# Kernel tuning notes

Measured on AMD Instinct MI355X. Metric: run time of the kernel, lower is better.

Reference implementation:

```python
import jax, jax.numpy as jnp
import numpy as np

N = 50_000          # nodes
E = 1_600_000       # edges (avg degree 32)
IN = 128            # in_feats
H = 4               # num_heads
F = 32              # out_feats per head
CUTOFF = 4.0        # bessel_cutoff
P = 7               # envelope_exponent + 1
ENV_A = -(P + 1) * (P + 2) / 2.0   # -36
ENV_B = P * (P + 2)                # 63
ENV_C = -P * (P + 1) / 2.0         # -28


def setup_inputs() -> dict:
    key = jax.random.key(0)
    ks = jax.random.split(key, 8)
    x = jax.random.normal(ks[0], (N, IN), dtype=jnp.float32)
    distance = jax.random.uniform(ks[1], (E,), dtype=jnp.float32) * CUTOFF
    W_src = jax.random.normal(ks[2], (H * F, IN), dtype=jnp.float32) * 0.05
    b_src = jnp.zeros((H * F,), dtype=jnp.float32)
    W_dst = jax.random.normal(ks[3], (H * F, IN), dtype=jnp.float32) * 0.05
    b_dst = jnp.zeros((H * F,), dtype=jnp.float32)
    attn = jax.random.normal(ks[4], (1, H, F), dtype=jnp.float32) * 0.1
    prelu_alpha = jnp.full((H,), 0.25, dtype=jnp.float32)
    frequencies = jnp.arange(1.0, H + 1.0, dtype=jnp.float32) * np.pi
    src = jax.random.randint(ks[5], (E,), 0, N, dtype=jnp.int32)
    dst = jax.random.randint(ks[6], (E,), 0, N, dtype=jnp.int32)
    return dict(x=x, distance=distance, W_src=W_src, b_src=b_src,
                W_dst=W_dst, b_dst=b_dst, attn=attn,
                prelu_alpha=prelu_alpha, frequencies=frequencies,
                src=src, dst=dst)


def _bessel_coeff(distance, frequencies):
    # distance: [E] -> d_scaled: [E,1]; frequencies: [H] -> coeff: [E,H]
    d = (distance / CUTOFF)[:, None]
    d_p0 = d ** P
    env = d + ENV_A * d_p0 + ENV_B * (d_p0 * d) + ENV_C * (d_p0 * d * d)
    return env * jnp.sin(frequencies * d)


def reference(x, distance, W_src, b_src, W_dst, b_dst, attn,
              prelu_alpha, frequencies, src, dst):
    n = x.shape[0]
    feat_src = (x @ W_src.T + b_src).reshape(n, H, F)   # [N,H,F]
    feat_dst = (x @ W_dst.T + b_dst).reshape(n, H, F)   # [N,H,F]

    coeff = _bessel_coeff(distance, frequencies)[:, :, None]  # [E,H,1]

    el = feat_src[src]                                  # [E,H,F] gather
    e = (el + feat_dst[dst]) * coeff                    # u_add_v then bessel scale
    e = jnp.where(e >= 0, e, prelu_alpha[None, :, None] * e)  # PReLU per head
    score = jnp.einsum('ehf,hf->eh', e, attn[0])        # [E,H]

    # edge softmax over incoming edges per dst node, per head
    seg_max = jax.ops.segment_max(score, dst, num_segments=n)        # [N,H]
    ex = jnp.exp(score - seg_max[dst])                               # [E,H]
    denom = jax.ops.segment_sum(ex, dst, num_segments=n)             # [N,H]
    a = ex / denom[dst]                                              # [E,H]

    # u_mul_e + scatter-sum aggregation
    msgs = el * a[:, :, None]                                        # [E,H,F]
    rst = jax.ops.segment_sum(msgs, dst, num_segments=n)             # [N,H,F]
    return rst
```

## Files before the change

### kernel.cpp

```cpp
#include <hip/hip_runtime.h>
#include <hip/hip_bf16.h>
#include <math.h>

#define N_NODES 50000
#define E_EDGES 1600000
#define HF 128
#define INV_CUTOFF 0.25f
#define ENV_A -36.0f
#define ENV_B 63.0f
#define ENV_C -28.0f

#define GEMM_BLOCKS ((N_NODES + 63) / 64)
#define REC_CAP 72
#define NBUCK 196
#define BUCK_CAP 8960
#define EPB 6250
#define SPLIT 4
#define LCAP 32

typedef __attribute__((ext_vector_type(8))) short bf16x8;
typedef __attribute__((ext_vector_type(4))) float f32x4;

__device__ __forceinline__ unsigned short f2bf(float f) {
  unsigned u = __float_as_uint(f);
  u += 0x7fffu + ((u >> 16) & 1u);
  return (unsigned short)(u >> 16);
}
__device__ __forceinline__ unsigned pack2(float lo, float hi) {
  return (unsigned)f2bf(lo) | ((unsigned)f2bf(hi) << 16);
}
__device__ __forceinline__ float2 up2(unsigned v) {
  return make_float2(__uint_as_float(v << 16), __uint_as_float(v & 0xffff0000u));
}

__device__ __forceinline__ float2 p2add(float2 a, float2 b) {
  return make_float2(a.x + b.x, a.y + b.y);
}
__device__ __forceinline__ float2 p2fma(float2 a, float2 b, float2 c) {
  return make_float2(fmaf(a.x, b.x, c.x), fmaf(a.y, b.y, c.y));
}
__device__ __forceinline__ float2 p2abs(float2 a) {
  return make_float2(fabsf(a.x), fabsf(a.y));
}
__device__ __forceinline__ float2 p2fmas(float s, float2 b, float2 c) {
  return make_float2(fmaf(s, b.x, c.x), fmaf(s, b.y, c.y));
}

__global__ __launch_bounds__(256) void phase1(
    const float* __restrict__ x, const float* __restrict__ Ws,
    const float* __restrict__ Wd,
    const float* __restrict__ bs, const float* __restrict__ bd,
    unsigned short* __restrict__ fs, float* __restrict__ fd,
    const int* __restrict__ dst, const int* __restrict__ src,
    const float* __restrict__ dist,
    int* __restrict__ bcursor, unsigned* __restrict__ bb_pay,
    unsigned char* __restrict__ bb_loc) {
  __shared__ __align__(16) char smem[65536];

  if (blockIdx.x < GEMM_BLOCKS) {
    unsigned short* wlds = (unsigned short*)smem;

    for (int i = threadIdx.x; i < 4096; i += 256) {
      const int n = i >> 4, c = i & 15;
      const float* Wp = ((n < 128) ? Ws : Wd) + (size_t)(n & 127) * HF + c * 8;
      const float4 v0 = *(const float4*)Wp;
      const float4 v1 = *(const float4*)(Wp + 4);
      uint4 pk;
      pk.x = pack2(v0.x, v0.y); pk.y = pack2(v0.z, v0.w);
      pk.z = pack2(v1.x, v1.y); pk.w = pack2(v1.z, v1.w);
      ((uint4*)wlds)[n * 16 + (c ^ (n & 15))] = pk;
    }

    const int lane = threadIdx.x & 63;
    const int wave = threadIdx.x >> 6;
    const int m = lane & 15;
    const int quad = lane >> 4;
    const int row = blockIdx.x * 64 + wave * 16 + m;
    const int rowc = (row < N_NODES) ? row : (N_NODES - 1);

    union { bf16x8 v; unsigned u[4]; } af[4];
    #pragma unroll
    for (int kt = 0; kt < 4; kt++) {
      const float* xp = x + (size_t)rowc * HF + kt * 32 + quad * 8;
      const float4 u0 = *(const float4*)xp;
      const float4 u1 = *(const float4*)(xp + 4);
      af[kt].u[0] = pack2(u0.x, u0.y); af[kt].u[1] = pack2(u0.z, u0.w);
      af[kt].u[2] = pack2(u1.x, u1.y); af[kt].u[3] = pack2(u1.z, u1.w);
    }

    __syncthreads();

    float accA[16][4];
    #pragma unroll
    for (int nt = 0; nt < 16; nt++) {
      const int nrow = nt * 16 + m;
      f32x4 acc = {0.f, 0.f, 0.f, 0.f};
      #pragma unroll
      for (int kt = 0; kt < 4; kt++) {
        const int pc = (kt * 4 + quad) ^ m;
        const bf16x8 bf = *(const bf16x8*)(wlds + (size_t)nrow * HF + pc * 8);
        acc = __builtin_amdgcn_mfma_f32_16x16x32_bf16(af[kt].v, bf, acc, 0, 0, 0);
      }
      accA[nt][0] = acc[0]; accA[nt][1] = acc[1];
      accA[nt][2] = acc[2]; accA[nt][3] = acc[3];
    }

    __syncthreads();
    unsigned short* fsS = wlds;
    float* fdS = (float*)(wlds + 64 * 136);

    const int rl0 = wave * 16 + quad * 4;
    #pragma unroll
    for (int nt = 0; nt < 16; nt++) {
      const int col = nt * 16 + m;
      if (col < 128) {
        const float bias = bs[col];
        #pragma unroll
        for (int r = 0; r < 4; r++)
          fsS[(rl0 + r) * 136 + col] = f2bf(accA[nt][r] + bias);
      } else {
        const float bias = bd[col - 128];
        #pragma unroll
        for (int r = 0; r < 4; r++)
          fdS[(rl0 + r) * 132 + (col - 128)] = accA[nt][r] + bias;
      }
    }
    __syncthreads();

    for (int c = threadIdx.x; c < 1024; c += 256) {
      const int r = c >> 4, off = (c & 15) * 8;
      const int gr = blockIdx.x * 64 + r;
      if (gr < N_NODES)
        *(uint4*)(fs + (size_t)gr * HF + off) = *(const uint4*)(fsS + r * 136 + off);
    }
    for (int c = threadIdx.x; c < 2048; c += 256) {
      const int r = c >> 5, off = (c & 31) * 4;
      const int gr = blockIdx.x * 64 + r;
      if (gr < N_NODES)
        *(float4*)(fd + (size_t)gr * HF + off) = *(const float4*)(fdS + r * 132 + off);
    }
  } else {
    unsigned* pay_s      = (unsigned*)smem;
    unsigned char* bkt_s = (unsigned char*)(smem + 25000);
    unsigned char* loc_s = (unsigned char*)(smem + 31250);
    int* hist = (int*)(smem + 37504);
    int* loff = hist + NBUCK;
    int* base = loff + NBUCK;
    int* cur  = base + NBUCK;

    const int bb = blockIdx.x - GEMM_BLOCKS;
    for (int t = threadIdx.x; t < NBUCK; t += 256) { hist[t] = 0; cur[t] = 0; }
    __syncthreads();
    const int lo = bb * EPB;
    for (int k = threadIdx.x; k < EPB; k += 256)
      atomicAdd(&hist[dst[lo + k] >> 8], 1);
    __syncthreads();
    if (threadIdx.x == 0) {
      int run = 0;
      for (int j = 0; j < NBUCK; j++) { loff[j] = run; run += hist[j]; }
    }
    __syncthreads();
    for (int t = threadIdx.x; t < NBUCK; t += 256)
      base[t] = atomicAdd(&bcursor[t], hist[t]);
    __syncthreads();
    for (int k = threadIdx.x; k < EPB; k += 256) {
      const int d = dst[lo + k];
      const int b = d >> 8;
      float ds = dist[lo + k] * (INV_CUTOFF * 65536.f);
      unsigned dq = (unsigned)(ds + 0.5f);
      if (dq > 65535u) dq = 65535u;
      const int s = loff[b] + atomicAdd(&cur[b], 1);
      pay_s[s] = (unsigned)src[lo + k] | (dq << 16);
      bkt_s[s] = (unsigned char)b;
      loc_s[s] = (unsigned char)(d & 255);
    }
    __syncthreads();
    for (int s = threadIdx.x; s < EPB; s += 256) {
      const int b = bkt_s[s];
      const int dest = base[b] + (s - loff[b]);
      if (dest < BUCK_CAP) {
        bb_pay[(size_t)b * BUCK_CAP + dest] = pay_s[s];
        bb_loc[(size_t)b * BUCK_CAP + dest] = loc_s[s];
      }
    }
  }
}

__global__ __launch_bounds__(256) void bucket_scatter(
    const int* __restrict__ bcursor, const unsigned* __restrict__ bb_pay,
    const unsigned char* __restrict__ bb_loc,
    int* __restrict__ counts, unsigned* __restrict__ rec) {
  __shared__ int cnt[256];
  __shared__ unsigned recS[256 * LCAP];
  cnt[threadIdx.x] = 0;
  __syncthreads();
  const int b = blockIdx.x / SPLIT;
  const int q = blockIdx.x - b * SPLIT;
  const int total = min(bcursor[b], BUCK_CAP);
  const int lo = (total * q) / SPLIT;
  const int hi = (total * (q + 1)) / SPLIT;
  const size_t base = (size_t)b * BUCK_CAP;
  for (int i = lo + threadIdx.x; i < hi; i += 256) {
    const unsigned pay = bb_pay[base + i];
    const int local = bb_loc[base + i];
    const int r = atomicAdd(&cnt[local], 1);
    if (r < LCAP) recS[local * LCAP + r] = pay;
  }
  __syncthreads();
  const int node = (b << 8) + (int)threadIdx.x;
  if (node < N_NODES) {
    const int cl = min(cnt[threadIdx.x], LCAP);
    if (cl > 0) {
      const int gbase = atomicAdd(&counts[node], cl);
      unsigned* dstp = rec + (size_t)node * REC_CAP;
      const unsigned* srcp = recS + threadIdx.x * LCAP;
      for (int k = 0; k < cl; k++) {
        const int pos = gbase + k;
        if (pos < REC_CAP) dstp[pos] = srcp[k];
      }
    }
  }
}

__global__ __launch_bounds__(256) void gat_agg(
    const unsigned short* __restrict__ fs, const float* __restrict__ fd,
    const int* __restrict__ counts, const unsigned* __restrict__ rec,
    const float* __restrict__ attn, const float* __restrict__ alpha_p,
    const float* __restrict__ freqs, float* __restrict__ out) {
  const int wave = threadIdx.x >> 6;
  const int lane = threadIdx.x & 63;
  const int node = blockIdx.x * 4 + wave;
  if (node >= N_NODES) return;
  const int eslot = lane >> 4;
  const int h = (lane >> 2) & 3;
  const int j = lane & 3;
  const int fo = (h << 5) + (j << 3);

  const float* fdp = fd + (size_t)node * HF + fo;
  const float2 f0 = *(const float2*)(fdp + 0);
  const float2 f1 = *(const float2*)(fdp + 2);
  const float2 f2 = *(const float2*)(fdp + 4);
  const float2 f3 = *(const float2*)(fdp + 6);
  const float2 t0 = *(const float2*)(attn + fo + 0);
  const float2 t1 = *(const float2*)(attn + fo + 2);
  const float2 t2 = *(const float2*)(attn + fo + 4);
  const float2 t3 = *(const float2*)(attn + fo + 6);
  const float al = alpha_p[h];
  const float c1 = 0.5f * (1.0f + al);
  const float c2 = 0.5f * (1.0f - al);
  const float fr = freqs[h];

  const int beg = node * REC_CAP;
  int cnt = counts[node];
  cnt = (cnt < REC_CAP) ? cnt : REC_CAP;
  const int end = beg + cnt;
  const unsigned short* fsp = fs + fo;

  float l = 0.f;
  float2 A0 = {0.f, 0.f}, A1 = {0.f, 0.f}, A2 = {0.f, 0.f}, A3 = {0.f, 0.f};

  for (int i = beg; i < end; i += 4) {
    const int e = i + eslot;
    const bool valid = (e < end);
    const unsigned r = rec[valid ? e : beg];
    const int s_idx = (int)(r & 0xffffu);
    const float d = (float)(r >> 16) * (1.0f / 65536.0f);
    const uint4 eb = *(const uint4*)(fsp + ((size_t)s_idx << 7));
    const float2 e0 = up2(eb.x);
    const float2 e1 = up2(eb.y);
    const float2 e2 = up2(eb.z);
    const float2 e3 = up2(eb.w);

    const float d2 = d * d;
    const float d4 = d2 * d2;
    const float d7 = d4 * d2 * d;
    const float env = fmaf(d7, fmaf(d, fmaf(d, ENV_C, ENV_B), ENV_A), d);
    const float cf = env * __sinf(fr * d);
    const float k1 = c1 * cf;
    const float k2 = c2 * fabsf(cf);

    float2 D1 = {0.f, 0.f}, D2 = {0.f, 0.f};
    float2 u;
    u = p2add(e0, f0); D1 = p2fma(u, t0, D1); D2 = p2fma(p2abs(u), t0, D2);
    u = p2add(e1, f1); D1 = p2fma(u, t1, D1); D2 = p2fma(p2abs(u), t1, D2);
    u = p2add(e2, f2); D1 = p2fma(u, t2, D1); D2 = p2fma(p2abs(u), t2, D2);
    u = p2add(e3, f3); D1 = p2fma(u, t3, D1); D2 = p2fma(p2abs(u), t3, D2);

    float p = fmaf(k1, D1.x + D1.y, k2 * (D2.x + D2.y));
    p += __shfl_xor(p, 1);
    p += __shfl_xor(p, 2);

    const float w = valid ? __expf(p) : 0.f;
    l += w;
    A0 = p2fmas(w, e0, A0);
    A1 = p2fmas(w, e1, A1);
    A2 = p2fmas(w, e2, A2);
    A3 = p2fmas(w, e3, A3);
  }

  #pragma unroll
  for (int mm = 16; mm < 64; mm <<= 1) {
    l    += __shfl_xor(l, mm);
    A0.x += __shfl_xor(A0.x, mm); A0.y += __shfl_xor(A0.y, mm);
    A1.x += __shfl_xor(A1.x, mm); A1.y += __shfl_xor(A1.y, mm);
    A2.x += __shfl_xor(A2.x, mm); A2.y += __shfl_xor(A2.y, mm);
    A3.x += __shfl_xor(A3.x, mm); A3.y += __shfl_xor(A3.y, mm);
  }

  if (eslot == 0) {
    const float rl = (l > 0.f) ? 1.0f / l : 0.f;
    float* o = out + (size_t)node * HF + fo;
    float4 o0 = {A0.x * rl, A0.y * rl, A1.x * rl, A1.y * rl};
    float4 o1 = {A2.x * rl, A2.y * rl, A3.x * rl, A3.y * rl};
    *(float4*)o = o0;
    *(float4*)(o + 4) = o1;
  }
}

extern "C" void kernel_launch(void* const* d_in, const int* in_sizes, int n_in,
                              void* d_out, int out_size, void* d_ws, size_t ws_size,
                              hipStream_t stream) {
  const float* x      = (const float*)d_in[0];
  const float* dist   = (const float*)d_in[1];
  const float* W_src  = (const float*)d_in[2];
  const float* b_src  = (const float*)d_in[3];
  const float* W_dst  = (const float*)d_in[4];
  const float* b_dst  = (const float*)d_in[5];
  const float* attn   = (const float*)d_in[6];
  const float* alpha  = (const float*)d_in[7];
  const float* freqs  = (const float*)d_in[8];
  const int*   src    = (const int*)d_in[9];
  const int*   dst    = (const int*)d_in[10];
  float* out = (float*)d_out;

  char* w = (char*)d_ws;
  size_t off = 0;
  auto alloc = [&](size_t bytes) -> void* {
    void* p = w + off;
    off += (bytes + 255) & ~(size_t)255;
    return p;
  };
  unsigned short* feat_src = (unsigned short*)alloc((size_t)N_NODES * HF * 2);
  float*          feat_dst = (float*)alloc((size_t)N_NODES * HF * 4);
  int*            counts   = (int*)alloc((size_t)N_NODES * 4);
  int*            bcursor  = (int*)alloc((size_t)NBUCK * 4);
  unsigned*       bb_pay   = (unsigned*)alloc((size_t)NBUCK * BUCK_CAP * 4);
  unsigned char*  bb_loc   = (unsigned char*)alloc((size_t)NBUCK * BUCK_CAP);
  unsigned*       rec      = (unsigned*)alloc((size_t)N_NODES * REC_CAP * 4);

  const size_t counts_pad = ((size_t)N_NODES * 4 + 255) & ~(size_t)255;
  hipMemsetAsync(counts, 0, counts_pad + (size_t)NBUCK * 4, stream);

  phase1<<<GEMM_BLOCKS + 256, 256, 0, stream>>>(
      x, W_src, W_dst, b_src, b_dst, feat_src, feat_dst,
      dst, src, dist, bcursor, bb_pay, bb_loc);

  bucket_scatter<<<NBUCK * SPLIT, 256, 0, stream>>>(bcursor, bb_pay, bb_loc, counts, rec);

  gat_agg<<<(N_NODES + 3) / 4, 256, 0, stream>>>(
      feat_src, feat_dst, counts, rec, attn, alpha, freqs, out);
}
```

Before: 244.0 us.

## Fuse bucket scatter into aggregation with 64-node buckets kept in shared memory

Shrinks dst buckets from 256 to 64 nodes and merges the bucket-scatter and aggregation kernels. Each 1024-thread block now bins its bucket's edges per node in shared memory and aggregates them directly, so the global per-node record array, its counts array and the memset of counts are no longer needed. The single-thread serial prefix over buckets in phase1 becomes a parallel block scan to cope with the larger bucket count. The cost is a smaller grid of large blocks with about 18KB of shared memory each, where each wave handles 4 nodes in sequence, which may lower latency hiding for the gathers.

```diff
diff --git a/kernel.cpp b/kernel.cpp
--- a/kernel.cpp
+++ b/kernel.cpp
@@ -12,11 +12,10 @@
 
 #define GEMM_BLOCKS ((N_NODES + 63) / 64)
 #define REC_CAP 72
-#define NBUCK 196
-#define BUCK_CAP 8960
+#define BNODES 64
+#define NBUCK 782
+#define BUCK_CAP 2560
 #define EPB 6250
-#define SPLIT 4
-#define LCAP 32
 
 typedef __attribute__((ext_vector_type(8))) short bf16x8;
 typedef __attribute__((ext_vector_type(4))) float f32x4;
@@ -141,23 +140,41 @@
     }
   } else {
     unsigned* pay_s      = (unsigned*)smem;
-    unsigned char* bkt_s = (unsigned char*)(smem + 25000);
-    unsigned char* loc_s = (unsigned char*)(smem + 31250);
-    int* hist = (int*)(smem + 37504);
+    unsigned short* bkt_s = (unsigned short*)(smem + 25000);
+    unsigned char* loc_s = (unsigned char*)(smem + 37500);
+    int* hist = (int*)(smem + 43752);
     int* loff = hist + NBUCK;
     int* base = loff + NBUCK;
     int* cur  = base + NBUCK;
+    int* part = cur + NBUCK;
 
     const int bb = blockIdx.x - GEMM_BLOCKS;
     for (int t = threadIdx.x; t < NBUCK; t += 256) { hist[t] = 0; cur[t] = 0; }
     __syncthreads();
     const int lo = bb * EPB;
     for (int k = threadIdx.x; k < EPB; k += 256)
-      atomicAdd(&hist[dst[lo + k] >> 8], 1);
-    __syncthreads();
-    if (threadIdx.x == 0) {
-      int run = 0;
-      for (int j = 0; j < NBUCK; j++) { loff[j] = run; run += hist[j]; }
+      atomicAdd(&hist[dst[lo + k] >> 6], 1);
+    __syncthreads();
+    int s = 0;
+    const int b0 = threadIdx.x * 4;
+    #pragma unroll
+    for (int k = 0; k < 4; k++) {
+      const int bi = b0 + k;
+      if (bi < NBUCK) s += hist[bi];
+    }
+    part[threadIdx.x] = s;
+    __syncthreads();
+    for (int offm = 1; offm < 256; offm <<= 1) {
+      const int v = (threadIdx.x >= offm) ? part[threadIdx.x - offm] : 0;
+      __syncthreads();
+      part[threadIdx.x] += v;
+      __syncthreads();
+    }
+    int run = part[threadIdx.x] - s;
+    #pragma unroll
+    for (int k = 0; k < 4; k++) {
+      const int bi = b0 + k;
+      if (bi < NBUCK) { loff[bi] = run; run += hist[bi]; }
     }
     __syncthreads();
     for (int t = threadIdx.x; t < NBUCK; t += 256)
@@ -165,82 +182,57 @@
     __syncthreads();
     for (int k = threadIdx.x; k < EPB; k += 256) {
       const int d = dst[lo + k];
-      const int b = d >> 8;
+      const int b = d >> 6;
       float ds = dist[lo + k] * (INV_CUTOFF * 65536.f);
       unsigned dq = (unsigned)(ds + 0.5f);
       if (dq > 65535u) dq = 65535u;
-      const int s = loff[b] + atomicAdd(&cur[b], 1);
-      pay_s[s] = (unsigned)src[lo + k] | (dq << 16);
-      bkt_s[s] = (unsigned char)b;
-      loc_s[s] = (unsigned char)(d & 255);
-    }
-    __syncthreads();
-    for (int s = threadIdx.x; s < EPB; s += 256) {
-      const int b = bkt_s[s];
-      const int dest = base[b] + (s - loff[b]);
+      const int sdx = loff[b] + atomicAdd(&cur[b], 1);
+      pay_s[sdx] = (unsigned)src[lo + k] | (dq << 16);
+      bkt_s[sdx] = (unsigned short)b;
+      loc_s[sdx] = (unsigned char)(d & 63);
+    }
+    __syncthreads();
+    for (int sdx = threadIdx.x; sdx < EPB; sdx += 256) {
+      const int b = bkt_s[sdx];
+      const int dest = base[b] + (sdx - loff[b]);
       if (dest < BUCK_CAP) {
-        bb_pay[(size_t)b * BUCK_CAP + dest] = pay_s[s];
-        bb_loc[(size_t)b * BUCK_CAP + dest] = loc_s[s];
+        bb_pay[(size_t)b * BUCK_CAP + dest] = pay_s[sdx];
+        bb_loc[(size_t)b * BUCK_CAP + dest] = loc_s[sdx];
       }
     }
   }
 }
 
-__global__ __launch_bounds__(256) void bucket_scatter(
+__global__ __launch_bounds__(1024) void bucket_agg(
+    const unsigned short* __restrict__ fs, const float* __restrict__ fd,
     const int* __restrict__ bcursor, const unsigned* __restrict__ bb_pay,
     const unsigned char* __restrict__ bb_loc,
-    int* __restrict__ counts, unsigned* __restrict__ rec) {
-  __shared__ int cnt[256];
-  __shared__ unsigned recS[256 * LCAP];
-  cnt[threadIdx.x] = 0;
+    const float* __restrict__ attn, const float* __restrict__ alpha_p,
+    const float* __restrict__ freqs, float* __restrict__ out) {
+  __shared__ int cnt[BNODES];
+  __shared__ unsigned recS[BNODES * REC_CAP];
+  const int b = blockIdx.x;
+
+  if (threadIdx.x < BNODES) cnt[threadIdx.x] = 0;
   __syncthreads();
-  const int b = blockIdx.x / SPLIT;
-  const int q = blockIdx.x - b * SPLIT;
+
   const int total = min(bcursor[b], BUCK_CAP);
-  const int lo = (total * q) / SPLIT;
-  const int hi = (total * (q + 1)) / SPLIT;
-  const size_t base = (size_t)b * BUCK_CAP;
-  for (int i = lo + threadIdx.x; i < hi; i += 256) {
-    const unsigned pay = bb_pay[base + i];
-    const int local = bb_loc[base + i];
+  const size_t bbase = (size_t)b * BUCK_CAP;
+  for (int i = threadIdx.x; i < total; i += 1024) {
+    const unsigned pay = bb_pay[bbase + i];
+    const int local = bb_loc[bbase + i];
     const int r = atomicAdd(&cnt[local], 1);
-    if (r < LCAP) recS[local * LCAP + r] = pay;
+    if (r < REC_CAP) recS[local * REC_CAP + r] = pay;
   }
   __syncthreads();
-  const int node = (b << 8) + (int)threadIdx.x;
-  if (node < N_NODES) {
-    const int cl = min(cnt[threadIdx.x], LCAP);
-    if (cl > 0) {
-      const int gbase = atomicAdd(&counts[node], cl);
-      unsigned* dstp = rec + (size_t)node * REC_CAP;
-      const unsigned* srcp = recS + threadIdx.x * LCAP;
-      for (int k = 0; k < cl; k++) {
-        const int pos = gbase + k;
-        if (pos < REC_CAP) dstp[pos] = srcp[k];
-      }
-    }
-  }
-}
-
-__global__ __launch_bounds__(256) void gat_agg(
-    const unsigned short* __restrict__ fs, const float* __restrict__ fd,
-    const int* __restrict__ counts, const unsigned* __restrict__ rec,
-    const float* __restrict__ attn, const float* __restrict__ alpha_p,
-    const float* __restrict__ freqs, float* __restrict__ out) {
+
   const int wave = threadIdx.x >> 6;
   const int lane = threadIdx.x & 63;
-  const int node = blockIdx.x * 4 + wave;
-  if (node >= N_NODES) return;
   const int eslot = lane >> 4;
   const int h = (lane >> 2) & 3;
   const int j = lane & 3;
   const int fo = (h << 5) + (j << 3);
 
-  const float* fdp = fd + (size_t)node * HF + fo;
-  const float2 f0 = *(const float2*)(fdp + 0);
-  const float2 f1 = *(const float2*)(fdp + 2);
-  const float2 f2 = *(const float2*)(fdp + 4);
-  const float2 f3 = *(const float2*)(fdp + 6);
   const float2 t0 = *(const float2*)(attn + fo + 0);
   const float2 t1 = *(const float2*)(attn + fo + 2);
   const float2 t2 = *(const float2*)(attn + fo + 4);
@@ -249,71 +241,83 @@
   const float c1 = 0.5f * (1.0f + al);
   const float c2 = 0.5f * (1.0f - al);
   const float fr = freqs[h];
-
-  const int beg = node * REC_CAP;
-  int cnt = counts[node];
-  cnt = (cnt < REC_CAP) ? cnt : REC_CAP;
-  const int end = beg + cnt;
   const unsigned short* fsp = fs + fo;
 
-  float l = 0.f;
-  float2 A0 = {0.f, 0.f}, A1 = {0.f, 0.f}, A2 = {0.f, 0.f}, A3 = {0.f, 0.f};
-
-  for (int i = beg; i < end; i += 4) {
-    const int e = i + eslot;
-    const bool valid = (e < end);
-    const unsigned r = rec[valid ? e : beg];
-    const int s_idx = (int)(r & 0xffffu);
-    const float d = (float)(r >> 16) * (1.0f / 65536.0f);
-    const uint4 eb = *(const uint4*)(fsp + ((size_t)s_idx << 7));
-    const float2 e0 = up2(eb.x);
-    const float2 e1 = up2(eb.y);
-    const float2 e2 = up2(eb.z);
-    const float2 e3 = up2(eb.w);
-
-    const float d2 = d * d;
-    const float d4 = d2 * d2;
-    const float d7 = d4 * d2 * d;
-    const float env = fmaf(d7, fmaf(d, fmaf(d, ENV_C, ENV_B), ENV_A), d);
-    const float cf = env * __sinf(fr * d);
-    const float k1 = c1 * cf;
-    const float k2 = c2 * fabsf(cf);
-
-    float2 D1 = {0.f, 0.f}, D2 = {0.f, 0.f};
-    float2 u;
-    u = p2add(e0, f0); D1 = p2fma(u, t0, D1); D2 = p2fma(p2abs(u), t0, D2);
-    u = p2add(e1, f1); D1 = p2fma(u, t1, D1); D2 = p2fma(p2abs(u), t1, D2);
-    u = p2add(e2, f2); D1 = p2fma(u, t2, D1); D2 = p2fma(p2abs(u), t2, D2);
-    u = p2add(e3, f3); D1 = p2fma(u, t3, D1); D2 = p2fma(p2abs(u), t3, D2);
-
-    float p = fmaf(k1, D1.x + D1.y, k2 * (D2.x + D2.y));
-    p += __shfl_xor(p, 1);
-    p += __shfl_xor(p, 2);
-
-    const float w = valid ? __expf(p) : 0.f;
-    l += w;
-    A0 = p2fmas(w, e0, A0);
-    A1 = p2fmas(w, e1, A1);
-    A2 = p2fmas(w, e2, A2);
-    A3 = p2fmas(w, e3, A3);
-  }
-
-  #pragma unroll
-  for (int mm = 16; mm < 64; mm <<= 1) {
-    l    += __shfl_xor(l, mm);
-    A0.x += __shfl_xor(A0.x, mm); A0.y += __shfl_xor(A0.y, mm);
-    A1.x += __shfl_xor(A1.x, mm); A1.y += __shfl_xor(A1.y, mm);
-    A2.x += __shfl_xor(A2.x, mm); A2.y += __shfl_xor(A2.y, mm);
-    A3.x += __shfl_xor(A3.x, mm); A3.y += __shfl_xor(A3.y, mm);
-  }
-
-  if (eslot == 0) {
-    const float rl = (l > 0.f) ? 1.0f / l : 0.f;
-    float* o = out + (size_t)node * HF + fo;
-    float4 o0 = {A0.x * rl, A0.y * rl, A1.x * rl, A1.y * rl};
-    float4 o1 = {A2.x * rl, A2.y * rl, A3.x * rl, A3.y * rl};
-    *(float4*)o = o0;
-    *(float4*)(o + 4) = o1;
+  #pragma unroll 1
+  for (int nn = 0; nn < 4; nn++) {
+    const int local = wave * 4 + nn;
+    const int node = b * BNODES + local;
+    if (node >= N_NODES) break;
+
+    int c = cnt[local];
+    c = (c < REC_CAP) ? c : REC_CAP;
+    const unsigned* recp = recS + local * REC_CAP;
+
+    const float* fdp = fd + (size_t)node * HF + fo;
+    const float2 f0 = *(const float2*)(fdp + 0);
+    const float2 f1 = *(const float2*)(fdp + 2);
+    const float2 f2 = *(const float2*)(fdp + 4);
+    const float2 f3 = *(const float2*)(fdp + 6);
+
+    float l = 0.f;
+    float2 A0 = {0.f, 0.f}, A1 = {0.f, 0.f}, A2 = {0.f, 0.f}, A3 = {0.f, 0.f};
+
+    for (int i = 0; i < c; i += 4) {
+      const int idx = i + eslot;
+      const bool valid = (idx < c);
+      const unsigned r = recp[valid ? idx : 0];
+      const int s_idx = (int)(r & 0xffffu);
+      const float d = (float)(r >> 16) * (1.0f / 65536.0f);
+      const uint4 eb = *(const uint4*)(fsp + ((size_t)s_idx << 7));
+      const float2 e0 = up2(eb.x);
+      const float2 e1 = up2(eb.y);
+      const float2 e2 = up2(eb.z);
+      const float2 e3 = up2(eb.w);
+
+      const float d2 = d * d;
+      const float d4 = d2 * d2;
+      const float d7 = d4 * d2 * d;
+      const float env = fmaf(d7, fmaf(d, fmaf(d, ENV_C, ENV_B), ENV_A), d);
+      const float cf = env * __sinf(fr * d);
+      const float k1 = c1 * cf;
+      const float k2 = c2 * fabsf(cf);
+
+      float2 D1 = {0.f, 0.f}, D2 = {0.f, 0.f};
+      float2 u;
+      u = p2add(e0, f0); D1 = p2fma(u, t0, D1); D2 = p2fma(p2abs(u), t0, D2);
+      u = p2add(e1, f1); D1 = p2fma(u, t1, D1); D2 = p2fma(p2abs(u), t1, D2);
+      u = p2add(e2, f2); D1 = p2fma(u, t2, D1); D2 = p2fma(p2abs(u), t2, D2);
+      u = p2add(e3, f3); D1 = p2fma(u, t3, D1); D2 = p2fma(p2abs(u), t3, D2);
+
+      float p = fmaf(k1, D1.x + D1.y, k2 * (D2.x + D2.y));
+      p += __shfl_xor(p, 1);
+      p += __shfl_xor(p, 2);
+
+      const float w = valid ? __expf(p) : 0.f;
+      l += w;
+      A0 = p2fmas(w, e0, A0);
+      A1 = p2fmas(w, e1, A1);
+      A2 = p2fmas(w, e2, A2);
+      A3 = p2fmas(w, e3, A3);
+    }
+
+    #pragma unroll
+    for (int mm = 16; mm < 64; mm <<= 1) {
+      l    += __shfl_xor(l, mm);
+      A0.x += __shfl_xor(A0.x, mm); A0.y += __shfl_xor(A0.y, mm);
+      A1.x += __shfl_xor(A1.x, mm); A1.y += __shfl_xor(A1.y, mm);
+      A2.x += __shfl_xor(A2.x, mm); A2.y += __shfl_xor(A2.y, mm);
+      A3.x += __shfl_xor(A3.x, mm); A3.y += __shfl_xor(A3.y, mm);
+    }
+
+    if (eslot == 0) {
+      const float rl = (l > 0.f) ? 1.0f / l : 0.f;
+      float* o = out + (size_t)node * HF + fo;
+      float4 o0 = {A0.x * rl, A0.y * rl, A1.x * rl, A1.y * rl};
+      float4 o1 = {A2.x * rl, A2.y * rl, A3.x * rl, A3.y * rl};
+      *(float4*)o = o0;
+      *(float4*)(o + 4) = o1;
+    }
   }
 }
 
@@ -342,21 +346,16 @@
   };
   unsigned short* feat_src = (unsigned short*)alloc((size_t)N_NODES * HF * 2);
   float*          feat_dst = (float*)alloc((size_t)N_NODES * HF * 4);
-  int*            counts   = (int*)alloc((size_t)N_NODES * 4);
   int*            bcursor  = (int*)alloc((size_t)NBUCK * 4);
   unsigned*       bb_pay   = (unsigned*)alloc((size_t)NBUCK * BUCK_CAP * 4);
   unsigned char*  bb_loc   = (unsigned char*)alloc((size_t)NBUCK * BUCK_CAP);
-  unsigned*       rec      = (unsigned*)alloc((size_t)N_NODES * REC_CAP * 4);
-
-  const size_t counts_pad = ((size_t)N_NODES * 4 + 255) & ~(size_t)255;
-  hipMemsetAsync(counts, 0, counts_pad + (size_t)NBUCK * 4, stream);
+
+  hipMemsetAsync(bcursor, 0, (size_t)NBUCK * 4, stream);
 
   phase1<<<GEMM_BLOCKS + 256, 256, 0, stream>>>(
       x, W_src, W_dst, b_src, b_dst, feat_src, feat_dst,
       dst, src, dist, bcursor, bb_pay, bb_loc);
 
-  bucket_scatter<<<NBUCK * SPLIT, 256, 0, stream>>>(bcursor, bb_pay, bb_loc, counts, rec);
-
-  gat_agg<<<(N_NODES + 3) / 4, 256, 0, stream>>>(
-      feat_src, feat_dst, counts, rec, attn, alpha, freqs, out);
-}
+  bucket_agg<<<NBUCK, 1024, 0, stream>>>(
+      feat_src, feat_dst, bcursor, bb_pay, bb_loc, attn, alpha, freqs, out);
+}
```

Result: slower. 253.3 us (+3.8%).

## Store feat_src head-major and pin each head to an XCD pair for aggregation

Applied to the files above, without the earlier changes.

The GEMM epilogue now writes bf16 source features in a head-major [H][N][32] layout. The aggregation kernel is restructured so each wave handles one (node, head) pair with 16 edges in flight. Block indices are mapped so blockIdx&7 selects the head and a half, which should keep each head's gather traffic on one pair of XCD L2 caches. The goal is better cache locality for the random source gathers, since each XCD's L2 only needs 1/4 of feat_src. In exchange the rec array and feat_dst are read four times per node, and the grid is four times larger.

```diff
diff --git a/kernel.cpp b/kernel.cpp
--- a/kernel.cpp
+++ b/kernel.cpp
@@ -50,7 +50,7 @@
     const float* __restrict__ x, const float* __restrict__ Ws,
     const float* __restrict__ Wd,
     const float* __restrict__ bs, const float* __restrict__ bd,
-    unsigned short* __restrict__ fs, float* __restrict__ fd,
+    unsigned short* __restrict__ fsh, float* __restrict__ fd,
     const int* __restrict__ dst, const int* __restrict__ src,
     const float* __restrict__ dist,
     int* __restrict__ bcursor, unsigned* __restrict__ bb_pay,
@@ -128,10 +128,12 @@
     __syncthreads();
 
     for (int c = threadIdx.x; c < 1024; c += 256) {
-      const int r = c >> 4, off = (c & 15) * 8;
+      const int r = c >> 4, off8 = (c & 15) * 8;
       const int gr = blockIdx.x * 64 + r;
+      const int hh = off8 >> 5, wf = off8 & 31;
       if (gr < N_NODES)
-        *(uint4*)(fs + (size_t)gr * HF + off) = *(const uint4*)(fsS + r * 136 + off);
+        *(uint4*)(fsh + ((size_t)hh * N_NODES + gr) * 32 + wf) =
+            *(const uint4*)(fsS + r * 136 + off8);
     }
     for (int c = threadIdx.x; c < 2048; c += 256) {
       const int r = c >> 5, off = (c & 31) * 4;
@@ -222,50 +224,52 @@
   }
 }
 
-__global__ __launch_bounds__(256) void gat_agg(
-    const unsigned short* __restrict__ fs, const float* __restrict__ fd,
+__global__ __launch_bounds__(256) void head_agg(
+    const unsigned short* __restrict__ fsh, const float* __restrict__ fd,
     const int* __restrict__ counts, const unsigned* __restrict__ rec,
     const float* __restrict__ attn, const float* __restrict__ alpha_p,
     const float* __restrict__ freqs, float* __restrict__ out) {
+  const int xcd = blockIdx.x & 7;
+  const int h = xcd >> 1;
+  const int half = xcd & 1;
+  const int g = blockIdx.x >> 3;
   const int wave = threadIdx.x >> 6;
+  const int node = (g * 2 + half) * 4 + wave;
   const int lane = threadIdx.x & 63;
-  const int node = blockIdx.x * 4 + wave;
-  if (node >= N_NODES) return;
-  const int eslot = lane >> 4;
-  const int h = (lane >> 2) & 3;
-  const int j = lane & 3;
-  const int fo = (h << 5) + (j << 3);
-
-  const float* fdp = fd + (size_t)node * HF + fo;
+  const int eslot = lane >> 2;
+  const int jj = lane & 3;
+  const int fo = jj * 8;
+
+  const float* fdp = fd + (size_t)node * HF + h * 32 + fo;
   const float2 f0 = *(const float2*)(fdp + 0);
   const float2 f1 = *(const float2*)(fdp + 2);
   const float2 f2 = *(const float2*)(fdp + 4);
   const float2 f3 = *(const float2*)(fdp + 6);
-  const float2 t0 = *(const float2*)(attn + fo + 0);
-  const float2 t1 = *(const float2*)(attn + fo + 2);
-  const float2 t2 = *(const float2*)(attn + fo + 4);
-  const float2 t3 = *(const float2*)(attn + fo + 6);
+  const float* tp = attn + h * 32 + fo;
+  const float2 t0 = *(const float2*)(tp + 0);
+  const float2 t1 = *(const float2*)(tp + 2);
+  const float2 t2 = *(const float2*)(tp + 4);
+  const float2 t3 = *(const float2*)(tp + 6);
   const float al = alpha_p[h];
   const float c1 = 0.5f * (1.0f + al);
   const float c2 = 0.5f * (1.0f - al);
   const float fr = freqs[h];
 
-  const int beg = node * REC_CAP;
   int cnt = counts[node];
   cnt = (cnt < REC_CAP) ? cnt : REC_CAP;
-  const int end = beg + cnt;
-  const unsigned short* fsp = fs + fo;
+  const int beg = node * REC_CAP;
+  const unsigned short* fp = fsh + (size_t)h * N_NODES * 32 + fo;
 
   float l = 0.f;
   float2 A0 = {0.f, 0.f}, A1 = {0.f, 0.f}, A2 = {0.f, 0.f}, A3 = {0.f, 0.f};
 
-  for (int i = beg; i < end; i += 4) {
-    const int e = i + eslot;
-    const bool valid = (e < end);
-    const unsigned r = rec[valid ? e : beg];
+  for (int i = 0; i < cnt; i += 16) {
+    const int idx = i + eslot;
+    const bool valid = (idx < cnt);
+    const unsigned r = rec[beg + (valid ? idx : 0)];
     const int s_idx = (int)(r & 0xffffu);
     const float d = (float)(r >> 16) * (1.0f / 65536.0f);
-    const uint4 eb = *(const uint4*)(fsp + ((size_t)s_idx << 7));
+    const uint4 eb = *(const uint4*)(fp + ((size_t)s_idx << 5));
     const float2 e0 = up2(eb.x);
     const float2 e1 = up2(eb.y);
     const float2 e2 = up2(eb.z);
@@ -299,7 +303,7 @@
   }
 
   #pragma unroll
-  for (int mm = 16; mm < 64; mm <<= 1) {
+  for (int mm = 4; mm <= 32; mm <<= 1) {
     l    += __shfl_xor(l, mm);
     A0.x += __shfl_xor(A0.x, mm); A0.y += __shfl_xor(A0.y, mm);
     A1.x += __shfl_xor(A1.x, mm); A1.y += __shfl_xor(A1.y, mm);
@@ -309,7 +313,7 @@
 
   if (eslot == 0) {
     const float rl = (l > 0.f) ? 1.0f / l : 0.f;
-    float* o = out + (size_t)node * HF + fo;
+    float* o = out + (size_t)node * HF + h * 32 + fo;
     float4 o0 = {A0.x * rl, A0.y * rl, A1.x * rl, A1.y * rl};
     float4 o1 = {A2.x * rl, A2.y * rl, A3.x * rl, A3.y * rl};
     *(float4*)o = o0;
@@ -357,6 +361,6 @@
 
   bucket_scatter<<<NBUCK * SPLIT, 256, 0, stream>>>(bcursor, bb_pay, bb_loc, counts, rec);
 
-  gat_agg<<<(N_NODES + 3) / 4, 256, 0, stream>>>(
+  head_agg<<<6250 * 8, 256, 0, stream>>>(
       feat_src, feat_dst, counts, rec, attn, alpha, freqs, out);
 }
```

Result: slower. 285.5 us (+17.0%).
